# Kernel tuning notes

Hardware: AMD Instinct MI355X
Metric: run time of the kernel (lower is better)

The kernel has to match this reference:

```python
import jax, jax.numpy as jnp
import numpy as np

F = 32          # final_feature_size
S = 256         # coordinate stride for key packing (coords < 251, offsets +-1)
SENT = 2 ** 30  # sentinel key > any real packed key
DELTAS = [dx * S * S + dy * S + dz
          for dx in (-1, 0, 1) for dy in (-1, 0, 1) for dz in (-1, 0, 1)]  # 27 kernel offsets


def setup_inputs() -> dict:
    rng = np.random.default_rng(0)
    T, per_frame, B, Npts = 16, 40000, 2, 400000
    # --- history sweep voxels: coords [t, x, y, z], t = global frame id ---
    t = np.repeat(np.arange(T, dtype=np.int32), per_frame)
    xyz = rng.integers(1, 251, size=(T * per_frame, 3), dtype=np.int32)
    keys = ((t.astype(np.int64) * S + xyz[:, 0]) * S + xyz[:, 1]) * S + xyz[:, 2]
    _, idx = np.unique(keys, return_index=True)  # ME quantization dedup
    t, xyz = t[idx], xyz[idx]
    n = t.shape[0]
    history_coordinates = np.concatenate([t[:, None], xyz], axis=1).astype(np.int32)
    history_batches = (t // (T // B)).astype(np.int32)  # scene id per voxel
    history_features = rng.standard_normal((n, 1)).astype(np.float32)
    # --- current scan query points ---
    b = rng.integers(0, B, size=Npts).astype(np.int32)
    qxyz = rng.integers(1, 251, size=(Npts, 3), dtype=np.int32)
    curr_coords = np.concatenate([b[:, None], qxyz], axis=1).astype(np.int32)
    points = np.concatenate([b[:, None].astype(np.float32),
                             qxyz.astype(np.float32),
                             rng.standard_normal((Npts, 1)).astype(np.float32)], axis=1)
    # --- params ---
    W_bb = (rng.standard_normal((27, 1, F)) * (2.0 / 27) ** 0.5).astype(np.float32)
    W_conv = (rng.standard_normal((27, F, F)) * (1.0 / (27 * F)) ** 0.5).astype(np.float32)
    return {
        'history_features': jnp.asarray(history_features),
        'points': jnp.asarray(points),
        'W_bb': jnp.asarray(W_bb),
        'W_conv': jnp.asarray(W_conv),
        'history_coordinates': jnp.asarray(history_coordinates),
        'history_batches': jnp.asarray(history_batches),
        'curr_coords': jnp.asarray(curr_coords),
    }


def pack4(c):
    c = c.astype(jnp.int32)
    return ((c[:, 0] * S + c[:, 1]) * S + c[:, 2]) * S + c[:, 3]


def sparse_conv(sorted_keys, table_feats, out_keys, W):
    """Minkowski-style sparse conv: gather neighbor at each of 27 offsets, matmul, scatter-add."""
    n = sorted_keys.shape[0]
    out = jnp.zeros((out_keys.shape[0], W.shape[2]), table_feats.dtype)
    for i, d in enumerate(DELTAS):
        nk = out_keys + d
        pos = jnp.clip(jnp.searchsorted(sorted_keys, nk), 0, n - 1)
        valid = (sorted_keys[pos] == nk)[:, None]
        g = jnp.where(valid, table_feats[pos], 0.0)
        out = out + g @ W[i]
    return out


def reference(history_features, points, W_bb, W_conv,
              history_coordinates, history_batches, curr_coords):
    n = history_features.shape[0]
    # ---- history backbone (stand-in: one sparse 3x3x3 conv, 1->F, time col as batch) ----
    keys_h = pack4(history_coordinates)
    order = jnp.argsort(keys_h)
    bb = sparse_conv(keys_h[order], history_features[order], keys_h, W_bb)  # [n, F]
    # ---- MinkowskiMaxPooling kernel [1000,1,1,1]: max over time per (b,x,y,z) ----
    pool_coords = jnp.concatenate([history_batches[:, None], history_coordinates[:, 1:4]], axis=1)
    keys_p = pack4(pool_coords)
    uk, inv = jnp.unique(keys_p, return_inverse=True, size=n, fill_value=SENT)  # sorted
    pooled = jax.ops.segment_max(bb, inv, num_segments=n)                        # [n, F]
    # ---- current_conv evaluated at (unique) query voxels, then slice back to points ----
    keys_q = pack4(curr_coords)
    m = keys_q.shape[0]
    uq, qinv = jnp.unique(keys_q, return_inverse=True, size=m, fill_value=SENT)
    conv_q = sparse_conv(uk, pooled, uq, W_conv)  # [m, F]
    ofield = conv_q[qinv]                          # TensorField slice: per-point features
    # ---- mode='update_point_features', preserve_feature==3 ----
    return jnp.concatenate([points[:, :4], ofield], axis=1)  # [Npts, 4+F]
```

## Files before the change

### kernel.cpp

```cpp
#include <hip/hip_runtime.h>
#include <stdint.h>


#define TPB 256
#define SCAN_WPT 8
typedef unsigned long long u64;
typedef unsigned int u32;
typedef unsigned short u16;

__device__ __forceinline__ u32 trans16(float x) {
    u32 b = __float_as_uint(x);
    u32 bf = (b + 0x7FFFu + ((b >> 16) & 1u)) >> 16;
    return ((bf & 0x8000u) ? (~bf) : (bf | 0x8000u)) & 0xFFFFu;
}
__device__ __forceinline__ float detrans16(u32 u) {
    u32 orig = (u & 0x8000u) ? (u & 0x7FFFu) : ((~u) & 0xFFFFu);
    return __uint_as_float(orig << 16);
}

__global__ void build_bitmaps_kernel(const int4* __restrict__ hc,
                                     const int* __restrict__ hb,
                                     int n,
                                     u64* __restrict__ hist_bm,
                                     u64* __restrict__ pool_bm,
                                     u64* __restrict__ multi_bm) {
    int j = blockIdx.x * blockDim.x + threadIdx.x;
    if (j >= n) return;
    int4 c = hc[j];
    int key = ((c.x * 256 + c.y) * 256 + c.z) * 256 + c.w;
    atomicOr(&hist_bm[key >> 6], 1ull << (key & 63));
    int pk = ((hb[j] * 256 + c.y) * 256 + c.z) * 256 + c.w;
    u64 bit = 1ull << (pk & 63);
    u64 old = atomicOr(&pool_bm[pk >> 6], bit);
    if (old & bit) atomicOr(&multi_bm[pk >> 6], bit);
}

__global__ void scan_sum_kernel(const u64* __restrict__ bm, u32* __restrict__ bsum) {
    __shared__ u32 s[TPB];
    int t = threadIdx.x;
    size_t base = ((size_t)blockIdx.x * TPB + t) * SCAN_WPT;
    u32 acc = 0;
#pragma unroll
    for (int i = 0; i < SCAN_WPT; i++) acc += __popcll(bm[base + i]);
    s[t] = acc; __syncthreads();
    for (int off = TPB / 2; off > 0; off >>= 1) {
        if (t < off) s[t] += s[t + off];
        __syncthreads();
    }
    if (t == 0) bsum[blockIdx.x] = s[0];
}

__global__ void scan_partials_kernel(u32* __restrict__ bsum, int count) {
    __shared__ u32 s[TPB];
    int t = threadIdx.x;
    int wpt = count >> 8;
    u32 v[8]; u32 acc = 0;
    for (int i = 0; i < wpt; i++) { v[i] = bsum[t * wpt + i]; acc += v[i]; }
    s[t] = acc; __syncthreads();
    for (int off = 1; off < TPB; off <<= 1) {
        u32 x = (t >= off) ? s[t - off] : 0;
        __syncthreads();
        s[t] += x;
        __syncthreads();
    }
    u32 run = s[t] - acc;
    for (int i = 0; i < wpt; i++) { bsum[t * wpt + i] = run; run += v[i]; }
}

__global__ void scan_apply_kernel(const u64* __restrict__ bm,
                                  const u32* __restrict__ bsum,
                                  u32* __restrict__ rank) {
    __shared__ u32 s[TPB];
    int t = threadIdx.x;
    size_t base = ((size_t)blockIdx.x * TPB + t) * SCAN_WPT;
    u32 pc[SCAN_WPT]; u32 acc = 0;
#pragma unroll
    for (int i = 0; i < SCAN_WPT; i++) { pc[i] = __popcll(bm[base + i]); acc += pc[i]; }
    s[t] = acc; __syncthreads();
    for (int off = 1; off < TPB; off <<= 1) {
        u32 x = (t >= off) ? s[t - off] : 0;
        __syncthreads();
        s[t] += x;
        __syncthreads();
    }
    u32 run = bsum[blockIdx.x] + s[t] - acc;
#pragma unroll
    for (int i = 0; i < SCAN_WPT; i++) { rank[base + i] = run; run += pc[i]; }
}

__global__ void zero_multi_kernel(const u64* __restrict__ multi_bm,
                                  const u64* __restrict__ pool_bm,
                                  const u32* __restrict__ pool_rank,
                                  u32* __restrict__ pooled) {
    int wI = blockIdx.x * blockDim.x + threadIdx.x;
    u64 mw = multi_bm[wI];
    if (!mw) return;
    u64 pw = pool_bm[wI];
    u32 rb = pool_rank[wI];
    while (mw) {
        int b = __ffsll((long long)mw) - 1;
        mw &= mw - 1;
        u32 slot = rb + (u32)__popcll(pw & ((1ull << b) - 1ull));
        u32* row = pooled + (size_t)slot * 16;
#pragma unroll
        for (int i = 0; i < 16; i++) row[i] = 0u;
    }
}

__global__ __launch_bounds__(TPB, 8)
void bb_pool_kernel(const int4* __restrict__ hc,
                    const int* __restrict__ hb,
                    const float* __restrict__ hf,
                    const float* __restrict__ Wbb,
                    int n,
                    const u64* __restrict__ hist_bm,
                    const u32* __restrict__ hist_rank,
                    const u64* __restrict__ pool_bm,
                    const u32* __restrict__ pool_rank,
                    const u64* __restrict__ multi_bm,
                    u32* __restrict__ pooled) {
    int nwg = gridDim.x;
    int q = nwg >> 3, r = nwg & 7;
    int xcd = blockIdx.x & 7, idx = blockIdx.x >> 3;
    int swz = (xcd < r ? xcd * (q + 1) : r * (q + 1) + (xcd - r) * q) + idx;

    int p = (swz * TPB + threadIdx.x) >> 5;
    if (p >= n) return;
    int lane = threadIdx.x & 63;
    int hb32 = lane & 32;
    int f = lane & 31;

    int4 c = hc[p];
    int key = ((c.x * 256 + c.y) * 256 + c.z) * 256 + c.w;
    int pk = ((hb[p] * 256 + c.y) * 256 + c.z) * 256 + c.w;

    u64 pword = pool_bm[pk >> 6];
    u32 prank = pool_rank[pk >> 6];
    u64 mword = multi_bm[pk >> 6];

    float fv = 0.f;
    bool hit = false;
    if (f < 27) {
        int t1 = f / 9, rem = f - t1 * 9, t2 = rem / 3, t3 = rem - t2 * 3;
        int nk = key + (t1 - 1) * 65536 + (t2 - 1) * 256 + (t3 - 1);
        u64 word = hist_bm[nk >> 6];
        u32 rk   = hist_rank[nk >> 6];
        if ((word >> (nk & 63)) & 1ull) {
            u32 r2 = rk + (u32)__popcll(word & ((1ull << (nk & 63)) - 1ull));
            fv = hf[r2];
            hit = true;
        }
    }
    unsigned long long bal = __ballot(hit);
    u32 mymask = (u32)(bal >> hb32);

    float acc = 0.f;
    while (mymask) {
        int b = __ffs(mymask) - 1;
        mymask &= mymask - 1;
        float fb = __shfl(fv, hb32 + b);
        acc = fmaf(fb, Wbb[b * 32 + f], acc);
    }

    int bit = pk & 63;
    int slot = (int)(prank + (u32)__popcll(pword & ((1ull << bit) - 1ull)));
    bool multi = (mword >> bit) & 1ull;

    u32 tv = trans16(acc);
    u32 packed = tv | (((u32)__shfl_down((int)tv, 1)) << 16);
    if ((f & 1) == 0) {
        u32* addr = pooled + (size_t)slot * 16 + (f >> 1);
        if (!multi) {
            *addr = packed;
        } else {
            u32 oldv = *addr;
            while (true) {
                u32 lo = max(oldv & 0xFFFFu, packed & 0xFFFFu);
                u32 hi = max(oldv >> 16, packed >> 16);
                u32 mx = lo | (hi << 16);
                if (mx == oldv) break;
                u32 prev = atomicCAS(addr, oldv, mx);
                if (prev == oldv) break;
                oldv = prev;
            }
        }
    }
}

__global__ __launch_bounds__(TPB, 8)
void query_kernel(const int4* __restrict__ qc,
                  const float* __restrict__ pts,
                  const float* __restrict__ Wc,
                  int m,
                  const u64* __restrict__ pool_bm,
                  const u32* __restrict__ pool_rank,
                  const u16* __restrict__ pooled16,
                  float* __restrict__ out) {
    int p = (blockIdx.x * blockDim.x + threadIdx.x) >> 5;
    if (p >= m) return;
    int lane = threadIdx.x & 63;
    int hb32 = lane & 32;
    int f = lane & 31;

    int4 c = qc[p];
    int qk = ((c.x * 256 + c.y) * 256 + c.z) * 256 + c.w;

    int slotL = -1;
    if (f < 27) {
        int t1 = f / 9, rem = f - t1 * 9, t2 = rem / 3, t3 = rem - t2 * 3;
        int nk = qk + (t1 - 1) * 65536 + (t2 - 1) * 256 + (t3 - 1);
        u64 word = pool_bm[nk >> 6];
        u32 rk   = pool_rank[nk >> 6];
        if ((word >> (nk & 63)) & 1ull)
            slotL = (int)(rk + (u32)__popcll(word & ((1ull << (nk & 63)) - 1ull)));
    }
    unsigned long long bal = __ballot(slotL >= 0);
    u32 mymask = (u32)(bal >> hb32);

    float acc = 0.f;
    while (mymask) {
        int b = __ffs(mymask) - 1;
        mymask &= mymask - 1;
        int slot = __shfl(slotL, hb32 + b);
        float pv = detrans16(pooled16[(size_t)slot * 32 + f]);
        const float* W = Wc + b * 1024 + f;
#pragma unroll
        for (int k = 0; k < 32; k++) {
            float pk_ = __shfl(pv, hb32 + k);
            acc = fmaf(pk_, W[k * 32], acc);
        }
    }

    float acc2 = __shfl_down(acc, 1);
    if ((f & 1) == 0) {
        float2 st; st.x = acc; st.y = acc2;
        *(float2*)(out + (size_t)p * 36 + 4 + f) = st;
    }
    if (f < 4) out[(size_t)p * 36 + f] = pts[p * 5 + f];
}

extern "C" void kernel_launch(void* const* d_in, const int* in_sizes, int n_in,
                              void* d_out, int out_size, void* d_ws, size_t ws_size,
                              hipStream_t stream) {
    const float* hfeat   = (const float*)d_in[0];
    const float* pts     = (const float*)d_in[1];
    const float* Wbb     = (const float*)d_in[2];
    const float* Wconv   = (const float*)d_in[3];
    const int4*  hcoords = (const int4*)d_in[4];
    const int*   hbatch  = (const int*)d_in[5];
    const int4*  qcoords = (const int4*)d_in[6];
    int n = in_sizes[0];
    int m = in_sizes[1] / 5;

    const int NW_H = 1 << 22;
    const int NW_P = 1 << 19;
    const int GB_H = NW_H / (TPB * SCAN_WPT);
    const int GB_P = NW_P / (TPB * SCAN_WPT);

    char* w = (char*)d_ws;
    char* zbase = w;
    u64* hist_bm      = (u64*)w;       w += (size_t)NW_H * 8;
    u64* pool_bm      = (u64*)w;       w += (size_t)NW_P * 8;
    u64* multi_bm     = (u64*)w;       w += (size_t)NW_P * 8;
    size_t zbytes = (size_t)(w - zbase);
    u32* pooled       = (u32*)w;       w += (size_t)n * 64;
    u32* hist_rank    = (u32*)w;       w += (size_t)NW_H * 4;
    u32* pool_rank    = (u32*)w;       w += (size_t)NW_P * 4;
    u32* bsum_h       = (u32*)w;       w += (size_t)GB_H * 4;
    u32* bsum_p       = (u32*)w;

    hipMemsetAsync(zbase, 0x00, zbytes, stream);

    int gb_n   = (n + TPB - 1) / TPB;
    int gb_n32 = (int)(((long long)n * 32 + TPB - 1) / TPB);
    int gb_m32 = (int)(((long long)m * 32 + TPB - 1) / TPB);

    build_bitmaps_kernel<<<gb_n, TPB, 0, stream>>>(hcoords, hbatch, n,
                                                   hist_bm, pool_bm, multi_bm);
    scan_sum_kernel<<<GB_H, TPB, 0, stream>>>(hist_bm, bsum_h);
    scan_partials_kernel<<<1, TPB, 0, stream>>>(bsum_h, GB_H);
    scan_apply_kernel<<<GB_H, TPB, 0, stream>>>(hist_bm, bsum_h, hist_rank);
    scan_sum_kernel<<<GB_P, TPB, 0, stream>>>(pool_bm, bsum_p);
    scan_partials_kernel<<<1, TPB, 0, stream>>>(bsum_p, GB_P);
    scan_apply_kernel<<<GB_P, TPB, 0, stream>>>(pool_bm, bsum_p, pool_rank);
    zero_multi_kernel<<<NW_P / TPB, TPB, 0, stream>>>(multi_bm, pool_bm,
                                                      pool_rank, pooled);
    bb_pool_kernel<<<gb_n32, TPB, 0, stream>>>(hcoords, hbatch, hfeat, Wbb, n,
                                               hist_bm, hist_rank,
                                               pool_bm, pool_rank, multi_bm, pooled);
    query_kernel<<<gb_m32, TPB, 0, stream>>>(qcoords, pts, Wconv, m,
                                             pool_bm, pool_rank,
                                             (const u16*)pooled, (float*)d_out);
}
```

Before: 279.7 us.

## Merge hist/pool scans into shared launches, fold zeroing, use ds_swizzle broadcast

Runs the hist and pool bitmap prefix scans together: one block-sum kernel covering both grids, one partials kernel that scans both bsum arrays, and one apply kernel. The multi-hit zeroing pass is folded into the pool half of the apply kernel. Together this cuts the kernel count from seven to three and removes small serial launches. The query kernel's 32-lane broadcast loop now uses ds_swizzle broadcast patterns instead of __shfl, aiming for cheaper cross-lane reads. The swizzle pattern assumes 32-lane groups, and GB_H and GB_P are now hardcoded constants.

```diff
diff --git a/kernel.cpp b/kernel.cpp
--- a/kernel.cpp
+++ b/kernel.cpp
@@ -1,9 +1,12 @@
 #include <hip/hip_runtime.h>
 #include <stdint.h>
+#include <utility>
 
 
 #define TPB 256
 #define SCAN_WPT 8
+#define GB_H 2048
+#define GB_P 256
 typedef unsigned long long u64;
 typedef unsigned int u32;
 typedef unsigned short u16;
@@ -16,6 +19,16 @@
 __device__ __forceinline__ float detrans16(u32 u) {
     u32 orig = (u & 0x8000u) ? (u & 0x7FFFu) : ((~u) & 0xFFFFu);
     return __uint_as_float(orig << 16);
+}
+
+template <int... Ks>
+__device__ __forceinline__ void kfma(float pv, const float* __restrict__ W,
+                                     float& acc,
+                                     std::integer_sequence<int, Ks...>) {
+    ((acc = fmaf(__uint_as_float((u32)__builtin_amdgcn_ds_swizzle(
+                     (int)__float_as_uint(pv), (Ks << 5))),
+                 W[Ks * 32], acc)),
+     ...);
 }
 
 __global__ void build_bitmaps_kernel(const int4* __restrict__ hc,
@@ -35,10 +48,15 @@
     if (old & bit) atomicOr(&multi_bm[pk >> 6], bit);
 }
 
-__global__ void scan_sum_kernel(const u64* __restrict__ bm, u32* __restrict__ bsum) {
+__global__ void scan_sum_all_kernel(const u64* __restrict__ hist_bm,
+                                    const u64* __restrict__ pool_bm,
+                                    u32* __restrict__ bsum) {
     __shared__ u32 s[TPB];
     int t = threadIdx.x;
-    size_t base = ((size_t)blockIdx.x * TPB + t) * SCAN_WPT;
+    bool isPool = blockIdx.x >= GB_H;
+    const u64* bm = isPool ? pool_bm : hist_bm;
+    int blk = isPool ? (blockIdx.x - GB_H) : blockIdx.x;
+    size_t base = ((size_t)blk * TPB + t) * SCAN_WPT;
     u32 acc = 0;
 #pragma unroll
     for (int i = 0; i < SCAN_WPT; i++) acc += __popcll(bm[base + i]);
@@ -50,12 +68,12 @@
     if (t == 0) bsum[blockIdx.x] = s[0];
 }
 
-__global__ void scan_partials_kernel(u32* __restrict__ bsum, int count) {
+__global__ void scan_partials_all_kernel(u32* __restrict__ bsum) {
     __shared__ u32 s[TPB];
     int t = threadIdx.x;
-    int wpt = count >> 8;
     u32 v[8]; u32 acc = 0;
-    for (int i = 0; i < wpt; i++) { v[i] = bsum[t * wpt + i]; acc += v[i]; }
+#pragma unroll
+    for (int i = 0; i < 8; i++) { v[i] = bsum[t * 8 + i]; acc += v[i]; }
     s[t] = acc; __syncthreads();
     for (int off = 1; off < TPB; off <<= 1) {
         u32 x = (t >= off) ? s[t - off] : 0;
@@ -64,15 +82,34 @@
         __syncthreads();
     }
     u32 run = s[t] - acc;
-    for (int i = 0; i < wpt; i++) { bsum[t * wpt + i] = run; run += v[i]; }
-}
-
-__global__ void scan_apply_kernel(const u64* __restrict__ bm,
-                                  const u32* __restrict__ bsum,
-                                  u32* __restrict__ rank) {
+#pragma unroll
+    for (int i = 0; i < 8; i++) { bsum[t * 8 + i] = run; run += v[i]; }
+    __syncthreads();
+    u32 pv = bsum[GB_H + t];
+    s[t] = pv; __syncthreads();
+    for (int off = 1; off < TPB; off <<= 1) {
+        u32 x = (t >= off) ? s[t - off] : 0;
+        __syncthreads();
+        s[t] += x;
+        __syncthreads();
+    }
+    bsum[GB_H + t] = s[t] - pv;
+}
+
+__global__ void scan_apply_all_kernel(const u64* __restrict__ hist_bm,
+                                      const u64* __restrict__ pool_bm,
+                                      const u32* __restrict__ bsum,
+                                      u32* __restrict__ hist_rank,
+                                      u32* __restrict__ pool_rank,
+                                      const u64* __restrict__ multi_bm,
+                                      u32* __restrict__ pooled) {
     __shared__ u32 s[TPB];
     int t = threadIdx.x;
-    size_t base = ((size_t)blockIdx.x * TPB + t) * SCAN_WPT;
+    bool isPool = blockIdx.x >= GB_H;
+    const u64* bm = isPool ? pool_bm : hist_bm;
+    u32* rank = isPool ? pool_rank : hist_rank;
+    int blk = isPool ? (blockIdx.x - GB_H) : blockIdx.x;
+    size_t base = ((size_t)blk * TPB + t) * SCAN_WPT;
     u32 pc[SCAN_WPT]; u32 acc = 0;
 #pragma unroll
     for (int i = 0; i < SCAN_WPT; i++) { pc[i] = __popcll(bm[base + i]); acc += pc[i]; }
@@ -84,26 +121,27 @@
         __syncthreads();
     }
     u32 run = bsum[blockIdx.x] + s[t] - acc;
+    u32 run0 = run;
 #pragma unroll
     for (int i = 0; i < SCAN_WPT; i++) { rank[base + i] = run; run += pc[i]; }
-}
-
-__global__ void zero_multi_kernel(const u64* __restrict__ multi_bm,
-                                  const u64* __restrict__ pool_bm,
-                                  const u32* __restrict__ pool_rank,
-                                  u32* __restrict__ pooled) {
-    int wI = blockIdx.x * blockDim.x + threadIdx.x;
-    u64 mw = multi_bm[wI];
-    if (!mw) return;
-    u64 pw = pool_bm[wI];
-    u32 rb = pool_rank[wI];
-    while (mw) {
-        int b = __ffsll((long long)mw) - 1;
-        mw &= mw - 1;
-        u32 slot = rb + (u32)__popcll(pw & ((1ull << b) - 1ull));
-        u32* row = pooled + (size_t)slot * 16;
-#pragma unroll
-        for (int i = 0; i < 16; i++) row[i] = 0u;
+    if (isPool) {
+        u32 r2 = run0;
+#pragma unroll
+        for (int i = 0; i < SCAN_WPT; i++) {
+            u64 mw = multi_bm[base + i];
+            if (mw) {
+                u64 pw = bm[base + i];
+                while (mw) {
+                    int b = __ffsll((long long)mw) - 1;
+                    mw &= mw - 1;
+                    u32 slot = r2 + (u32)__popcll(pw & ((1ull << b) - 1ull));
+                    u32* row = pooled + (size_t)slot * 16;
+#pragma unroll
+                    for (int w2 = 0; w2 < 16; w2++) row[w2] = 0u;
+                }
+            }
+            r2 += pc[i];
+        }
     }
 }
 
@@ -224,11 +262,7 @@
         int slot = __shfl(slotL, hb32 + b);
         float pv = detrans16(pooled16[(size_t)slot * 32 + f]);
         const float* W = Wc + b * 1024 + f;
-#pragma unroll
-        for (int k = 0; k < 32; k++) {
-            float pk_ = __shfl(pv, hb32 + k);
-            acc = fmaf(pk_, W[k * 32], acc);
-        }
+        kfma(pv, W, acc, std::make_integer_sequence<int, 32>{});
     }
 
     float acc2 = __shfl_down(acc, 1);
@@ -254,8 +288,6 @@
 
     const int NW_H = 1 << 22;
     const int NW_P = 1 << 19;
-    const int GB_H = NW_H / (TPB * SCAN_WPT);
-    const int GB_P = NW_P / (TPB * SCAN_WPT);
 
     char* w = (char*)d_ws;
     char* zbase = w;
@@ -266,8 +298,7 @@
     u32* pooled       = (u32*)w;       w += (size_t)n * 64;
     u32* hist_rank    = (u32*)w;       w += (size_t)NW_H * 4;
     u32* pool_rank    = (u32*)w;       w += (size_t)NW_P * 4;
-    u32* bsum_h       = (u32*)w;       w += (size_t)GB_H * 4;
-    u32* bsum_p       = (u32*)w;
+    u32* bsum         = (u32*)w;       w += (size_t)(GB_H + GB_P) * 4;
 
     hipMemsetAsync(zbase, 0x00, zbytes, stream);
 
@@ -277,14 +308,11 @@
 
     build_bitmaps_kernel<<<gb_n, TPB, 0, stream>>>(hcoords, hbatch, n,
                                                    hist_bm, pool_bm, multi_bm);
-    scan_sum_kernel<<<GB_H, TPB, 0, stream>>>(hist_bm, bsum_h);
-    scan_partials_kernel<<<1, TPB, 0, stream>>>(bsum_h, GB_H);
-    scan_apply_kernel<<<GB_H, TPB, 0, stream>>>(hist_bm, bsum_h, hist_rank);
-    scan_sum_kernel<<<GB_P, TPB, 0, stream>>>(pool_bm, bsum_p);
-    scan_partials_kernel<<<1, TPB, 0, stream>>>(bsum_p, GB_P);
-    scan_apply_kernel<<<GB_P, TPB, 0, stream>>>(pool_bm, bsum_p, pool_rank);
-    zero_multi_kernel<<<NW_P / TPB, TPB, 0, stream>>>(multi_bm, pool_bm,
-                                                      pool_rank, pooled);
+    scan_sum_all_kernel<<<GB_H + GB_P, TPB, 0, stream>>>(hist_bm, pool_bm, bsum);
+    scan_partials_all_kernel<<<1, TPB, 0, stream>>>(bsum);
+    scan_apply_all_kernel<<<GB_H + GB_P, TPB, 0, stream>>>(hist_bm, pool_bm, bsum,
+                                                           hist_rank, pool_rank,
+                                                           multi_bm, pooled);
     bb_pool_kernel<<<gb_n32, TPB, 0, stream>>>(hcoords, hbatch, hfeat, Wbb, n,
                                                hist_bm, hist_rank,
                                                pool_bm, pool_rank, multi_bm, pooled);
```

Measured after the change: 262.5 us. 6.2% less time.
